# Kernel tuning notes

Hardware: AMD Instinct MI355X
Metric: run time of the kernel (lower is better)

## Reference

```python
import jax, jax.numpy as jnp
import numpy as np

N_NODES = 100000
N_EDGES = 1600000
N_GRAPHS = 128
IN_F, H_F, OUT_F, HID, NCLS = 128, 128, 64, 10, 10

def setup_inputs() -> dict:
    key = jax.random.key(0)
    ks = jax.random.split(key, 12)
    feats = jax.random.normal(ks[0], (N_NODES, IN_F), dtype=jnp.float32)
    src = jax.random.randint(ks[1], (N_EDGES,), 0, N_NODES, dtype=jnp.int32)
    dst = jax.random.randint(ks[2], (N_EDGES,), 0, N_NODES, dtype=jnp.int32)
    graph_ids = jnp.sort(jax.random.randint(ks[3], (N_NODES,), 0, N_GRAPHS, dtype=jnp.int32))
    def glorot(k, shape):
        fan = shape[0] + shape[1]
        return jax.random.normal(k, shape, dtype=jnp.float32) * jnp.sqrt(2.0 / fan)
    return {
        'feats': feats, 'src': src, 'dst': dst, 'graph_ids': graph_ids,
        'W1': glorot(ks[4], (IN_F, H_F)), 'b1': jnp.zeros((H_F,), jnp.float32),
        'W2': glorot(ks[5], (H_F, OUT_F)), 'b2': jnp.zeros((OUT_F,), jnp.float32),
        'fcW1': glorot(ks[6], (OUT_F, HID)), 'fcb1': jnp.zeros((HID,), jnp.float32),
        'fcW2': glorot(ks[7], (HID, NCLS)), 'fcb2': jnp.zeros((NCLS,), jnp.float32),
    }

def _graph_conv(x, W, b, src, dst):
    # DGL GraphConv, norm='both': D_dst^{-1/2} A D_src^{-1/2} X W + b
    ones = jnp.ones((src.shape[0],), x.dtype)
    deg_out = jnp.clip(jax.ops.segment_sum(ones, src, num_segments=N_NODES), 1.0)
    deg_in = jnp.clip(jax.ops.segment_sum(ones, dst, num_segments=N_NODES), 1.0)
    x = x * jax.lax.rsqrt(deg_out)[:, None]
    m = jax.ops.segment_sum(x[src], dst, num_segments=N_NODES)  # gather-scatter over edges
    m = m * jax.lax.rsqrt(deg_in)[:, None]
    return m @ W + b

def reference(feats, src, dst, graph_ids, W1, b1, W2, b2, fcW1, fcb1, fcW2, fcb2):
    h = jax.nn.relu(_graph_conv(feats, W1, b1, src, dst))
    h = jax.nn.relu(_graph_conv(h, W2, b2, src, dst))
    # dgl.mean_nodes: per-graph mean pooling
    sums = jax.ops.segment_sum(h, graph_ids, num_segments=N_GRAPHS)
    counts = jnp.clip(jax.ops.segment_sum(jnp.ones((N_NODES,), h.dtype), graph_ids, num_segments=N_GRAPHS), 1.0)
    pooled = sums / counts[:, None]  # [G, OUT_F]
    z = jax.nn.relu(pooled @ fcW1 + fcb1)
    return jax.nn.softmax(z @ fcW2 + fcb2, axis=1)
```

## Files before the change

kernel.cpp:

```cpp
#include <hip/hip_runtime.h>
#include <hip/hip_bf16.h>

#define N_NODES 100000
#define N_EDGES 1600000
#define N_GRAPHS 128
#define IN_F 128
#define H_F 128
#define OUT_F 64
#define HID 10
#define NCLS 10
#define XPAD 136
#define BSH 7
#define NBUCK 782
#define SBLK 128
#define EPB (N_EDGES / SBLK)
#define NB_PREP 4
#define PCHUNK 8

typedef __attribute__((ext_vector_type(8))) short bf16x8;
typedef __attribute__((ext_vector_type(4))) float f32x4;
typedef __attribute__((ext_vector_type(2))) float f32x2;

__device__ __forceinline__ float bl(unsigned int u) { return __uint_as_float(u << 16); }
__device__ __forceinline__ float bh(unsigned int u) { return __uint_as_float(u & 0xffff0000u); }

__global__ __launch_bounds__(1024) void k_hist2(const int* __restrict__ src, const int* __restrict__ dst,
                                                int* __restrict__ Pd, int* __restrict__ Ps,
                                                const float* __restrict__ W1, const float* __restrict__ W2,
                                                unsigned short* __restrict__ Wt1, unsigned short* __restrict__ Wt2) {
    __shared__ int hd[NBUCK];
    __shared__ int hs[NBUCK];
    const int blk = blockIdx.x;
    if (blk < SBLK) {
        for (int i = threadIdx.x; i < NBUCK; i += 1024) { hd[i] = 0; hs[i] = 0; }
        __syncthreads();
        const int base = blk * EPB;
        for (int i = threadIdx.x; i < EPB; i += 1024) {
            atomicAdd(&hd[dst[base + i] >> BSH], 1);
            atomicAdd(&hs[src[base + i] >> BSH], 1);
        }
        __syncthreads();
        for (int b = threadIdx.x; b < NBUCK; b += 1024) {
            Pd[b * SBLK + blk] = hd[b];
            Ps[b * SBLK + blk] = hs[b];
        }
    } else {
        int t = (blk - SBLK) * 1024 + threadIdx.x;
        const int stride = NB_PREP * 1024;
        for (int i = t; i < 128 * 128; i += stride) {
            int c = i >> 7, k = i & 127;
            __hip_bfloat16 v = __float2bfloat16(W1[k * 128 + c]);
            Wt1[i] = *(unsigned short*)&v;
        }
        for (int i = t; i < 64 * 128; i += stride) {
            int c = i >> 7, k = i & 127;
            __hip_bfloat16 v = __float2bfloat16(W2[k * 64 + c]);
            Wt2[i] = *(unsigned short*)&v;
        }
    }
}

__global__ __launch_bounds__(SBLK) void k_scanA(int* __restrict__ Pd, int* __restrict__ Ps,
                                                int* __restrict__ Td, int* __restrict__ Ts) {
    __shared__ int sc[SBLK];
    const int b = blockIdx.x;
    const int t = threadIdx.x;
    int* P = (b < NBUCK) ? Pd : Ps;
    int* T = (b < NBUCK) ? Td : Ts;
    const int bb = (b < NBUCK) ? b : b - NBUCK;
    int v = P[bb * SBLK + t];
    sc[t] = v;
    __syncthreads();
    for (int off = 1; off < SBLK; off <<= 1) {
        int u = (t >= off) ? sc[t - off] : 0;
        __syncthreads();
        sc[t] += u;
        __syncthreads();
    }
    P[bb * SBLK + t] = sc[t] - v;
    if (t == SBLK - 1) T[bb] = sc[SBLK - 1];
}

__global__ __launch_bounds__(1024) void k_scanB(const int* __restrict__ Td, const int* __restrict__ Ts,
                                                int* __restrict__ Bd, int* __restrict__ Bs) {
    __shared__ int sc[1024];
    const int t = threadIdx.x;
    int v = (t < NBUCK) ? Td[t] : 0;
    sc[t] = v;
    __syncthreads();
    for (int off = 1; off < 1024; off <<= 1) {
        int u = (t >= off) ? sc[t - off] : 0;
        __syncthreads();
        sc[t] += u;
        __syncthreads();
    }
    if (t < NBUCK) Bd[t] = sc[t] - v;
    if (t == NBUCK - 1) Bd[NBUCK] = sc[t];
    __syncthreads();
    int v2 = (t < NBUCK) ? Ts[t] : 0;
    sc[t] = v2;
    __syncthreads();
    for (int off = 1; off < 1024; off <<= 1) {
        int u = (t >= off) ? sc[t - off] : 0;
        __syncthreads();
        sc[t] += u;
        __syncthreads();
    }
    if (t < NBUCK) Bs[t] = sc[t] - v2;
    if (t == NBUCK - 1) Bs[NBUCK] = sc[t];
}

__global__ __launch_bounds__(1024) void k_scatter(const int* __restrict__ src, const int* __restrict__ dst,
                                                  const int* __restrict__ Pd, const int* __restrict__ Ps,
                                                  const int* __restrict__ Bd, const int* __restrict__ Bs,
                                                  unsigned int* __restrict__ pb, unsigned char* __restrict__ sb) {
    __shared__ int tk[NBUCK];
    const int b = blockIdx.x;
    const bool isPb = b < SBLK;
    const int blk = isPb ? b : b - SBLK;
    if (isPb) {
        for (int i = threadIdx.x; i < NBUCK; i += 1024) tk[i] = Bd[i] + Pd[i * SBLK + blk];
    } else {
        for (int i = threadIdx.x; i < NBUCK; i += 1024) tk[i] = Bs[i] + Ps[i * SBLK + blk];
    }
    __syncthreads();
    const int base = blk * EPB;
    if (isPb) {
        for (int i = threadIdx.x; i < EPB; i += 1024) {
            int d = dst[base + i];
            int s = src[base + i];
            int bd = d >> BSH;
            int pos = atomicAdd(&tk[bd], 1);
            pb[pos] = ((unsigned)s << 7) | (unsigned)(d & 127);
        }
    } else {
        for (int i = threadIdx.x; i < EPB; i += 1024) {
            int s = src[base + i];
            int bs = s >> BSH;
            int pos = atomicAdd(&tk[bs], 1);
            sb[pos] = (unsigned char)(s & 127);
        }
    }
}

__global__ __launch_bounds__(256) void k_finalize(const unsigned int* __restrict__ pb, const int* __restrict__ Bd,
                                                  const unsigned char* __restrict__ sb, const int* __restrict__ Bs,
                                                  int* __restrict__ rp, int* __restrict__ cnt_out,
                                                  int* __restrict__ cols) {
    __shared__ int cnt[128];
    __shared__ int exc[128];
    __shared__ int tick[128];
    __shared__ int h[128];
    __shared__ int sc[128];
    const int b = blockIdx.x;
    const int tid = threadIdx.x;
    if (tid < 128) { cnt[tid] = 0; tick[tid] = 0; h[tid] = 0; }
    __syncthreads();
    const int e0 = Bd[b], e1 = Bd[b + 1];
    for (int i = e0 + tid; i < e1; i += 256) atomicAdd(&cnt[pb[i] & 127], 1);
    const int f0 = Bs[b], f1 = Bs[b + 1];
    for (int i = f0 + tid; i < f1; i += 256) atomicAdd(&h[sb[i]], 1);
    __syncthreads();
    if (tid < 128) sc[tid] = cnt[tid];
    __syncthreads();
    for (int off = 1; off < 128; off <<= 1) {
        int u = (tid < 128 && tid >= off) ? sc[tid - off] : 0;
        __syncthreads();
        if (tid < 128) sc[tid] += u;
        __syncthreads();
    }
    if (tid < 128) exc[tid] = sc[tid] - cnt[tid];
    __syncthreads();
    const int node0 = b << BSH;
    if (tid < 128 && node0 + tid < N_NODES) {
        rp[node0 + tid] = e0 + exc[tid];
        cnt_out[node0 + tid] = h[tid];
    }
    if (b == NBUCK - 1 && tid == 0) rp[N_NODES] = N_EDGES;
    for (int i = e0 + tid; i < e1; i += 256) {
        unsigned int p = pb[i];
        int loc = p & 127;
        int t = atomicAdd(&tick[loc], 1);
        cols[e0 + exc[loc] + t] = (int)(p >> 7);
    }
}

__global__ __launch_bounds__(256) void k_gemm1(const float* __restrict__ X,
                                               const unsigned short* __restrict__ Wt,
                                               const int* __restrict__ cnt_out,
                                               unsigned char* __restrict__ Gout) {
    __shared__ __align__(16) unsigned short Xs[32 * XPAD];
    __shared__ __align__(16) unsigned short Ws[128 * XPAD];
    const int tid = threadIdx.x;
    const int row0 = blockIdx.x * 32;

    {
        const float4* X4 = (const float4*)X;
#pragma unroll
        for (int j = 0; j < 4; j++) {
            int i = tid + 256 * j;
            int r = i >> 5, k4 = i & 31;
            float4 x = X4[(size_t)(row0 + r) * 32 + k4];
            __hip_bfloat162 lo = __float22bfloat162_rn({x.x, x.y});
            __hip_bfloat162 hi = __float22bfloat162_rn({x.z, x.w});
            uint2 u;
            u.x = *(unsigned int*)&lo;
            u.y = *(unsigned int*)&hi;
            *(uint2*)&Xs[r * XPAD + k4 * 4] = u;
        }
    }
    {
        const uint2* W2 = (const uint2*)Wt;
#pragma unroll
        for (int j = 0; j < 16; j++) {
            int i = tid + 256 * j;
            int cc = i >> 5, kk = i & 31;
            uint2 u = W2[(size_t)cc * 32 + kk];
            *(uint2*)&Ws[cc * XPAD + kk * 4] = u;
        }
    }
    __syncthreads();

    const int lane = tid & 63;
    const int wv = tid >> 6;
    const int m = lane & 15;
    const int q = lane >> 4;
    const int cg = wv * 32;

    f32x4 acc00 = {0.f, 0.f, 0.f, 0.f}, acc01 = {0.f, 0.f, 0.f, 0.f};
    f32x4 acc10 = {0.f, 0.f, 0.f, 0.f}, acc11 = {0.f, 0.f, 0.f, 0.f};
#pragma unroll
    for (int ks = 0; ks < 4; ks++) {
        int kb = ks * 32 + q * 8;
        bf16x8 a0 = *(const bf16x8*)&Xs[m * XPAD + kb];
        bf16x8 a1 = *(const bf16x8*)&Xs[(16 + m) * XPAD + kb];
        bf16x8 b0 = *(const bf16x8*)&Ws[(cg + m) * XPAD + kb];
        bf16x8 b1 = *(const bf16x8*)&Ws[(cg + 16 + m) * XPAD + kb];
        acc00 = __builtin_amdgcn_mfma_f32_16x16x32_bf16(a0, b0, acc00, 0, 0, 0);
        acc01 = __builtin_amdgcn_mfma_f32_16x16x32_bf16(a0, b1, acc01, 0, 0, 0);
        acc10 = __builtin_amdgcn_mfma_f32_16x16x32_bf16(a1, b0, acc10, 0, 0, 0);
        acc11 = __builtin_amdgcn_mfma_f32_16x16x32_bf16(a1, b1, acc11, 0, 0, 0);
    }
#pragma unroll
    for (int r = 0; r < 4; r++) {
        int rowA = row0 + q * 4 + r;
        int rowB = rowA + 16;
        float sA = rsqrtf((float)max(cnt_out[rowA], 1));
        float sB = rsqrtf((float)max(cnt_out[rowB], 1));
        unsigned int pkA = __builtin_amdgcn_cvt_pk_fp8_f32(acc00[r] * sA, acc01[r] * sA, 0, false);
        unsigned int pkB = __builtin_amdgcn_cvt_pk_fp8_f32(acc10[r] * sB, acc11[r] * sB, 0, false);
        unsigned char* gA = Gout + (size_t)rowA * 128 + cg + m;
        gA[0]  = (unsigned char)(pkA & 0xffu);
        gA[16] = (unsigned char)((pkA >> 8) & 0xffu);
        unsigned char* gB = Gout + (size_t)rowB * 128 + cg + m;
        gB[0]  = (unsigned char)(pkB & 0xffu);
        gB[16] = (unsigned char)((pkB >> 8) & 0xffu);
    }
}

template <int TOTF, bool XBF16, bool OUT_FP8>
__global__ __launch_bounds__(256) void k_gemm_mfma(const void* __restrict__ Xv,
                                                   const unsigned short* __restrict__ Wt,
                                                   const int* __restrict__ cnt_out,
                                                   void* __restrict__ GoutV) {
    __shared__ __align__(16) unsigned short Xs[32 * XPAD];
    __shared__ __align__(16) unsigned short Ws[64 * XPAD];
    const int tid = threadIdx.x;
    const int cbase = blockIdx.y * 64;
    const int row0 = blockIdx.x * 32;

    if constexpr (XBF16) {
        const uint2* X2 = (const uint2*)Xv;
#pragma unroll
        for (int j = 0; j < 4; j++) {
            int i = tid + 256 * j;
            int r = i >> 5, kk = i & 31;
            uint2 u = X2[(size_t)(row0 + r) * 32 + kk];
            *(uint2*)&Xs[r * XPAD + kk * 4] = u;
        }
    } else {
        const float4* X4 = (const float4*)Xv;
#pragma unroll
        for (int j = 0; j < 4; j++) {
            int i = tid + 256 * j;
            int r = i >> 5, k4 = i & 31;
            float4 x = X4[(size_t)(row0 + r) * 32 + k4];
            __hip_bfloat162 lo = __float22bfloat162_rn({x.x, x.y});
            __hip_bfloat162 hi = __float22bfloat162_rn({x.z, x.w});
            uint2 u;
            u.x = *(unsigned int*)&lo;
            u.y = *(unsigned int*)&hi;
            *(uint2*)&Xs[r * XPAD + k4 * 4] = u;
        }
    }
    {
        const uint2* W2 = (const uint2*)Wt;
#pragma unroll
        for (int j = 0; j < 8; j++) {
            int i = tid + 256 * j;
            int c = i >> 5, kk = i & 31;
            uint2 u = W2[(size_t)(cbase + c) * 32 + kk];
            *(uint2*)&Ws[c * XPAD + kk * 4] = u;
        }
    }
    __syncthreads();

    const int lane = tid & 63;
    const int wv = tid >> 6;
    const int m = lane & 15;
    const int q = lane >> 4;
    const int roff = (wv & 1) * 16;
    const int coff = (wv >> 1) * 32;

    f32x4 acc0 = {0.f, 0.f, 0.f, 0.f}, acc1 = {0.f, 0.f, 0.f, 0.f};
#pragma unroll
    for (int ks = 0; ks < 4; ks++) {
        int kb = ks * 32 + q * 8;
        bf16x8 a  = *(const bf16x8*)&Xs[(roff + m) * XPAD + kb];
        bf16x8 b0 = *(const bf16x8*)&Ws[(coff + m) * XPAD + kb];
        bf16x8 b1 = *(const bf16x8*)&Ws[(coff + 16 + m) * XPAD + kb];
        acc0 = __builtin_amdgcn_mfma_f32_16x16x32_bf16(a, b0, acc0, 0, 0, 0);
        acc1 = __builtin_amdgcn_mfma_f32_16x16x32_bf16(a, b1, acc1, 0, 0, 0);
    }
#pragma unroll
    for (int r = 0; r < 4; r++) {
        int row = row0 + roff + q * 4 + r;
        float s = rsqrtf((float)max(cnt_out[row], 1));
        int col0 = cbase + coff + m;
        if constexpr (OUT_FP8) {
            unsigned int pk = __builtin_amdgcn_cvt_pk_fp8_f32(acc0[r] * s, acc1[r] * s, 0, false);
            unsigned char* gp = (unsigned char*)GoutV + (size_t)row * TOTF + col0;
            gp[0]  = (unsigned char)(pk & 0xffu);
            gp[16] = (unsigned char)((pk >> 8) & 0xffu);
        } else {
            unsigned short* Gout = (unsigned short*)GoutV;
            __hip_bfloat16 o0 = __float2bfloat16(acc0[r] * s);
            __hip_bfloat16 o1 = __float2bfloat16(acc1[r] * s);
            Gout[(size_t)row * TOTF + col0]      = *(unsigned short*)&o0;
            Gout[(size_t)row * TOTF + col0 + 16] = *(unsigned short*)&o1;
        }
    }
}

__device__ __forceinline__ void tail128(const unsigned short* __restrict__ gl, const int* __restrict__ cols,
                                        int b, int d, int j, f32x2& acc) {
    while (j + 16 <= d) {
        unsigned int u[16];
#pragma unroll
        for (int k = 0; k < 16; k++) { int s = cols[b + j + k]; u[k] = gl[(size_t)s * 64]; }
#pragma unroll
        for (int k = 0; k < 16; k++) acc += __builtin_amdgcn_cvt_pk_f32_fp8(u[k], false);
        j += 16;
    }
    if (j + 8 <= d) {
        unsigned int u[8];
#pragma unroll
        for (int k = 0; k < 8; k++) { int s = cols[b + j + k]; u[k] = gl[(size_t)s * 64]; }
#pragma unroll
        for (int k = 0; k < 8; k++) acc += __builtin_amdgcn_cvt_pk_f32_fp8(u[k], false);
        j += 8;
    }
    if (j + 4 <= d) {
        unsigned int u[4];
#pragma unroll
        for (int k = 0; k < 4; k++) { int s = cols[b + j + k]; u[k] = gl[(size_t)s * 64]; }
#pragma unroll
        for (int k = 0; k < 4; k++) acc += __builtin_amdgcn_cvt_pk_f32_fp8(u[k], false);
        j += 4;
    }
    if (j + 2 <= d) {
        unsigned int u0, u1;
        { int s = cols[b + j];     u0 = gl[(size_t)s * 64]; }
        { int s = cols[b + j + 1]; u1 = gl[(size_t)s * 64]; }
        acc += __builtin_amdgcn_cvt_pk_f32_fp8(u0, false);
        acc += __builtin_amdgcn_cvt_pk_f32_fp8(u1, false);
        j += 2;
    }
    if (j < d) {
        int s = cols[b + j];
        unsigned int u = gl[(size_t)s * 64];
        acc += __builtin_amdgcn_cvt_pk_f32_fp8(u, false);
    }
}

__device__ __forceinline__ void tail64(const unsigned char* __restrict__ gl, const int* __restrict__ cols,
                                       int b, int d, int j, f32x2& acc) {
    while (j + 16 <= d) {
        unsigned int u[16];
#pragma unroll
        for (int k = 0; k < 16; k++) { int s = cols[b + j + k]; u[k] = gl[(size_t)s * 64]; }
#pragma unroll
        for (int k = 0; k < 16; k++) acc += __builtin_amdgcn_cvt_pk_f32_fp8(u[k], false);
        j += 16;
    }
    if (j + 8 <= d) {
        unsigned int u[8];
#pragma unroll
        for (int k = 0; k < 8; k++) { int s = cols[b + j + k]; u[k] = gl[(size_t)s * 64]; }
#pragma unroll
        for (int k = 0; k < 8; k++) acc += __builtin_amdgcn_cvt_pk_f32_fp8(u[k], false);
        j += 8;
    }
    if (j + 4 <= d) {
        unsigned int u[4];
#pragma unroll
        for (int k = 0; k < 4; k++) { int s = cols[b + j + k]; u[k] = gl[(size_t)s * 64]; }
#pragma unroll
        for (int k = 0; k < 4; k++) acc += __builtin_amdgcn_cvt_pk_f32_fp8(u[k], false);
        j += 4;
    }
    if (j + 2 <= d) {
        unsigned int u0, u1;
        { int s = cols[b + j];     u0 = gl[(size_t)s * 64]; }
        { int s = cols[b + j + 1]; u1 = gl[(size_t)s * 64]; }
        acc += __builtin_amdgcn_cvt_pk_f32_fp8(u0, false);
        acc += __builtin_amdgcn_cvt_pk_f32_fp8(u1, false);
        j += 2;
    }
    if (j < d) {
        int s = cols[b + j];
        unsigned int u = gl[(size_t)s * 64];
        acc += __builtin_amdgcn_cvt_pk_f32_fp8(u, false);
    }
}

__global__ __launch_bounds__(256) void k_spmm128f8(const unsigned short* __restrict__ G,
                                                   const int* __restrict__ rp,
                                                   const int* __restrict__ cols,
                                                   const float* __restrict__ bias,
                                                   unsigned int* __restrict__ H) {
    const int lane = threadIdx.x & 63;
    const int wave = threadIdx.x >> 6;
    const int v0 = (blockIdx.x * 4 + wave) * 2;
    const int b0 = __builtin_amdgcn_readfirstlane(rp[v0]);
    const int b1 = __builtin_amdgcn_readfirstlane(rp[v0 + 1]);
    const int e1 = __builtin_amdgcn_readfirstlane(rp[v0 + 2]);
    const int dA = b1 - b0, dB = e1 - b1;
    const unsigned short* gl = G + lane;
    f32x2 aA = {0.f, 0.f}, aB = {0.f, 0.f};
    int ja = 0, jb = 0;
    while (ja + 8 <= dA && jb + 8 <= dB) {
        unsigned int u[8], w[8];
#pragma unroll
        for (int k = 0; k < 8; k++) { int s = cols[b0 + ja + k]; u[k] = gl[(size_t)s * 64]; }
#pragma unroll
        for (int k = 0; k < 8; k++) { int s = cols[b1 + jb + k]; w[k] = gl[(size_t)s * 64]; }
#pragma unroll
        for (int k = 0; k < 8; k++) aA += __builtin_amdgcn_cvt_pk_f32_fp8(u[k], false);
#pragma unroll
        for (int k = 0; k < 8; k++) aB += __builtin_amdgcn_cvt_pk_f32_fp8(w[k], false);
        ja += 8; jb += 8;
    }
    tail128(gl, cols, b0, dA, ja, aA);
    tail128(gl, cols, b1, dB, jb, aB);

    {
        const float rs = rsqrtf((float)max(dA, 1));
        const float2 bb = *(const float2*)&bias[2 * lane];
        __hip_bfloat162 p = __float22bfloat162_rn({fmaxf(fmaf(aA.x, rs, bb.x), 0.f),
                                                   fmaxf(fmaf(aA.y, rs, bb.y), 0.f)});
        H[(size_t)v0 * 64 + lane] = *(unsigned int*)&p;
    }
    {
        const float rs = rsqrtf((float)max(dB, 1));
        const float2 bb = *(const float2*)&bias[2 * lane];
        __hip_bfloat162 p = __float22bfloat162_rn({fmaxf(fmaf(aB.x, rs, bb.x), 0.f),
                                                   fmaxf(fmaf(aB.y, rs, bb.y), 0.f)});
        H[(size_t)(v0 + 1) * 64 + lane] = *(unsigned int*)&p;
    }
}

__global__ __launch_bounds__(256) void k_spmm64f8(const unsigned char* __restrict__ G,
                                                  const int* __restrict__ rp,
                                                  const int* __restrict__ cols,
                                                  const float* __restrict__ bias,
                                                  unsigned short* __restrict__ H) {
    const int lane = threadIdx.x & 63;
    const int wave = threadIdx.x >> 6;
    const int v0 = (blockIdx.x * 4 + wave) * 2;
    const int b0 = __builtin_amdgcn_readfirstlane(rp[v0]);
    const int b1 = __builtin_amdgcn_readfirstlane(rp[v0 + 1]);
    const int e1 = __builtin_amdgcn_readfirstlane(rp[v0 + 2]);
    const int dA = b1 - b0, dB = e1 - b1;
    const unsigned char* gl = G + lane;
    f32x2 aA = {0.f, 0.f}, aB = {0.f, 0.f};
    int ja = 0, jb = 0;
    while (ja + 8 <= dA && jb + 8 <= dB) {
        unsigned int u[8], w[8];
#pragma unroll
        for (int k = 0; k < 8; k++) { int s = cols[b0 + ja + k]; u[k] = gl[(size_t)s * 64]; }
#pragma unroll
        for (int k = 0; k < 8; k++) { int s = cols[b1 + jb + k]; w[k] = gl[(size_t)s * 64]; }
#pragma unroll
        for (int k = 0; k < 8; k++) aA += __builtin_amdgcn_cvt_pk_f32_fp8(u[k], false);
#pragma unroll
        for (int k = 0; k < 8; k++) aB += __builtin_amdgcn_cvt_pk_f32_fp8(w[k], false);
        ja += 8; jb += 8;
    }
    tail64(gl, cols, b0, dA, ja, aA);
    tail64(gl, cols, b1, dB, jb, aB);

    {
        const float rs = rsqrtf((float)max(dA, 1));
        __hip_bfloat16 o = __float2bfloat16(fmaxf(fmaf(aA.x, rs, bias[lane]), 0.f));
        H[(size_t)v0 * 64 + lane] = *(unsigned short*)&o;
    }
    {
        const float rs = rsqrtf((float)max(dB, 1));
        __hip_bfloat16 o = __float2bfloat16(fmaxf(fmaf(aB.x, rs, bias[lane]), 0.f));
        H[(size_t)(v0 + 1) * 64 + lane] = *(unsigned short*)&o;
    }
}

__global__ __launch_bounds__(256) void k_pool(const unsigned short* __restrict__ h2,
                                              const int* __restrict__ gid,
                                              float* __restrict__ part) {
    __shared__ int se[2];
    __shared__ float red[16][16][4];
    const int cpart = blockIdx.x;
    const int g = blockIdx.y;
    const int tid = threadIdx.x;
    if (tid < 2) {
        int target = g + tid;
        int lo = 0, hi = N_NODES;
        while (lo < hi) {
            int mid = (lo + hi) >> 1;
            if (gid[mid] < target) lo = mid + 1; else hi = mid;
        }
        se[tid] = lo;
    }
    __syncthreads();
    const int s = se[0], e = se[1];
    const int chunk = (e - s + PCHUNK - 1) / PCHUNK;
    const int lo = s + cpart * chunk;
    const int hi = min(lo + chunk, e);
    const int r = tid >> 4, cp = tid & 15;
    float a0 = 0.f, a1 = 0.f, a2 = 0.f, a3 = 0.f;
    const uint2* H = (const uint2*)h2;
    for (int v = lo + r; v < hi; v += 16) {
        uint2 u = H[(size_t)v * 16 + cp];
        a0 += bl(u.x); a1 += bh(u.x); a2 += bl(u.y); a3 += bh(u.y);
    }
    red[r][cp][0] = a0; red[r][cp][1] = a1; red[r][cp][2] = a2; red[r][cp][3] = a3;
    for (int off = 8; off > 0; off >>= 1) {
        __syncthreads();
        if (r < off) {
#pragma unroll
            for (int k = 0; k < 4; k++) red[r][cp][k] += red[r + off][cp][k];
        }
    }
    __syncthreads();
    if (r == 0) {
        float4 o = {red[0][cp][0], red[0][cp][1], red[0][cp][2], red[0][cp][3]};
        *(float4*)&part[((size_t)cpart * N_GRAPHS + g) * 64 + 4 * cp] = o;
    }
}

__global__ __launch_bounds__(64) void k_mlp(const float* __restrict__ part,
                                            const int* __restrict__ gid,
                                            const float* __restrict__ fcW1,
                                            const float* __restrict__ fcb1,
                                            const float* __restrict__ fcW2,
                                            const float* __restrict__ fcb2,
                                            float* __restrict__ out) {
    __shared__ int se[2];
    __shared__ float p[64];
    __shared__ float z[10];
    __shared__ float l[10];
    __shared__ float red[2];
    const int g = blockIdx.x;
    const int t = threadIdx.x;
    if (t < 2) {
        int target = g + t;
        int lo = 0, hi = N_NODES;
        while (lo < hi) {
            int mid = (lo + hi) >> 1;
            if (gid[mid] < target) lo = mid + 1; else hi = mid;
        }
        se[t] = lo;
    }
    __syncthreads();
    const int cnt = max(se[1] - se[0], 1);
    float a = 0.f;
#pragma unroll
    for (int c = 0; c < PCHUNK; c++) a += part[((size_t)c * N_GRAPHS + g) * 64 + t];
    p[t] = a / (float)cnt;
    __syncthreads();
    if (t < 10) {
        float acc = fcb1[t];
        for (int k = 0; k < 64; k++) acc = fmaf(p[k], fcW1[k * 10 + t], acc);
        z[t] = fmaxf(acc, 0.f);
    }
    __syncthreads();
    if (t < 10) {
        float acc = fcb2[t];
        for (int k = 0; k < 10; k++) acc = fmaf(z[k], fcW2[k * 10 + t], acc);
        l[t] = acc;
    }
    __syncthreads();
    if (t == 0) {
        float m = l[0];
        for (int i = 1; i < 10; i++) m = fmaxf(m, l[i]);
        float ssum = 0.f;
        for (int i = 0; i < 10; i++) ssum += expf(l[i] - m);
        red[0] = m;
        red[1] = ssum;
    }
    __syncthreads();
    if (t < 10) out[g * 10 + t] = expf(l[t] - red[0]) / red[1];
}

extern "C" void kernel_launch(void* const* d_in, const int* in_sizes, int n_in,
                              void* d_out, int out_size, void* d_ws, size_t ws_size,
                              hipStream_t stream) {
    const float* feats = (const float*)d_in[0];
    const int* src = (const int*)d_in[1];
    const int* dst = (const int*)d_in[2];
    const int* gid = (const int*)d_in[3];
    const float* W1 = (const float*)d_in[4];
    const float* b1 = (const float*)d_in[5];
    const float* W2 = (const float*)d_in[6];
    const float* b2 = (const float*)d_in[7];
    const float* fcW1 = (const float*)d_in[8];
    const float* fcb1 = (const float*)d_in[9];
    const float* fcW2 = (const float*)d_in[10];
    const float* fcb2 = (const float*)d_in[11];
    float* out = (float*)d_out;

    char* w = (char*)d_ws;
    size_t off = 0;
    auto alloc = [&](size_t bytes) -> void* {
        void* p = w + off;
        off = (off + bytes + 255) & ~(size_t)255;
        return p;
    };
    int* cnt_out = (int*)alloc(N_NODES * 4);
    int* rp      = (int*)alloc((N_NODES + 1) * 4);
    int* cols    = (int*)alloc((size_t)N_EDGES * 4);
    int* Pd      = (int*)alloc(NBUCK * SBLK * 4);
    int* Ps      = (int*)alloc(NBUCK * SBLK * 4);
    int* Td      = (int*)alloc(NBUCK * 4);
    int* Ts      = (int*)alloc(NBUCK * 4);
    int* Bd      = (int*)alloc((NBUCK + 1) * 4);
    int* Bs      = (int*)alloc((NBUCK + 1) * 4);
    unsigned int* pb  = (unsigned int*)alloc((size_t)N_EDGES * 4);
    unsigned char* sb = (unsigned char*)alloc((size_t)N_EDGES);
    unsigned short* Wt1 = (unsigned short*)alloc(128 * 128 * 2);
    unsigned short* Wt2 = (unsigned short*)alloc(64 * 128 * 2);
    unsigned char* g1 = (unsigned char*)alloc((size_t)N_NODES * 128);
    unsigned short* h1 = (unsigned short*)alloc((size_t)N_NODES * 128 * 2);
    unsigned char* g2 = (unsigned char*)alloc((size_t)N_NODES * 64);
    unsigned short* h2 = (unsigned short*)alloc((size_t)N_NODES * 64 * 2);
    float* part = (float*)alloc((size_t)PCHUNK * N_GRAPHS * 64 * 4);

    k_hist2<<<SBLK + NB_PREP, 1024, 0, stream>>>(src, dst, Pd, Ps, W1, W2, Wt1, Wt2);
    k_scanA<<<2 * NBUCK, SBLK, 0, stream>>>(Pd, Ps, Td, Ts);
    k_scanB<<<1, 1024, 0, stream>>>(Td, Ts, Bd, Bs);
    k_scatter<<<2 * SBLK, 1024, 0, stream>>>(src, dst, Pd, Ps, Bd, Bs, pb, sb);
    k_finalize<<<NBUCK, 256, 0, stream>>>(pb, Bd, sb, Bs, rp, cnt_out, cols);

    k_gemm1<<<N_NODES / 32, 256, 0, stream>>>(feats, Wt1, cnt_out, g1);
    k_spmm128f8<<<N_NODES / 8, 256, 0, stream>>>((const unsigned short*)g1, rp, cols, b1, (unsigned int*)h1);

    k_gemm_mfma<64, true, true><<<dim3(N_NODES / 32, 1), 256, 0, stream>>>(h1, Wt2, cnt_out, g2);
    k_spmm64f8<<<N_NODES / 8, 256, 0, stream>>>(g2, rp, cols, b2, (unsigned short*)h2);

    k_pool<<<dim3(PCHUNK, N_GRAPHS), 256, 0, stream>>>(h2, gid, part);
    k_mlp<<<N_GRAPHS, 64, 0, stream>>>(part, gid, fcW1, fcb1, fcW2, fcb2, out);
}
```

Measured before the change: 260.5 us.

## Fuse mean-pool partial sums into layer-2 SpMM with atomics

The second SpMM kernel now reduces its eight output rows per block into per-graph sums in shared memory and atomically adds them into a single fp32 partial buffer. This removes the bf16 h2 write and read and the separate pooling kernel launch. The partial buffer is zeroed in the first prep kernel. The cost is 12500 blocks issuing float atomics onto a small buffer, which adds contention and makes the summation order nondeterministic.

```diff
diff --git a/kernel.cpp b/kernel.cpp
--- a/kernel.cpp
+++ b/kernel.cpp
@@ -15,7 +15,6 @@
 #define SBLK 128
 #define EPB (N_EDGES / SBLK)
 #define NB_PREP 4
-#define PCHUNK 8
 
 typedef __attribute__((ext_vector_type(8))) short bf16x8;
 typedef __attribute__((ext_vector_type(4))) float f32x4;
@@ -27,7 +26,8 @@
 __global__ __launch_bounds__(1024) void k_hist2(const int* __restrict__ src, const int* __restrict__ dst,
                                                 int* __restrict__ Pd, int* __restrict__ Ps,
                                                 const float* __restrict__ W1, const float* __restrict__ W2,
-                                                unsigned short* __restrict__ Wt1, unsigned short* __restrict__ Wt2) {
+                                                unsigned short* __restrict__ Wt1, unsigned short* __restrict__ Wt2,
+                                                float* __restrict__ part) {
     __shared__ int hd[NBUCK];
     __shared__ int hs[NBUCK];
     const int blk = blockIdx.x;
@@ -57,6 +57,7 @@
             __hip_bfloat16 v = __float2bfloat16(W2[k * 64 + c]);
             Wt2[i] = *(unsigned short*)&v;
         }
+        for (int i = t; i < N_GRAPHS * 64; i += stride) part[i] = 0.f;
     }
 }
 
@@ -474,15 +475,20 @@
                                                   const int* __restrict__ rp,
                                                   const int* __restrict__ cols,
                                                   const float* __restrict__ bias,
-                                                  unsigned short* __restrict__ H) {
+                                                  const int* __restrict__ gid,
+                                                  float* __restrict__ part) {
+    __shared__ float acc[8][64];
+    __shared__ int gv[8];
     const int lane = threadIdx.x & 63;
     const int wave = threadIdx.x >> 6;
-    const int v0 = (blockIdx.x * 4 + wave) * 2;
+    const int vb = blockIdx.x * 8;
+    const int v0 = vb + wave * 2;
     const int b0 = __builtin_amdgcn_readfirstlane(rp[v0]);
     const int b1 = __builtin_amdgcn_readfirstlane(rp[v0 + 1]);
     const int e1 = __builtin_amdgcn_readfirstlane(rp[v0 + 2]);
     const int dA = b1 - b0, dB = e1 - b1;
     const unsigned char* gl = G + lane;
+    if (threadIdx.x < 8) gv[threadIdx.x] = gid[vb + threadIdx.x];
     f32x2 aA = {0.f, 0.f}, aB = {0.f, 0.f};
     int ja = 0, jb = 0;
     while (ja + 8 <= dA && jb + 8 <= dB) {
@@ -500,59 +506,33 @@
     tail64(gl, cols, b0, dA, ja, aA);
     tail64(gl, cols, b1, dB, jb, aB);
 
+    const float bbias = bias[lane];
     {
         const float rs = rsqrtf((float)max(dA, 1));
-        __hip_bfloat16 o = __float2bfloat16(fmaxf(fmaf(aA.x, rs, bias[lane]), 0.f));
-        H[(size_t)v0 * 64 + lane] = *(unsigned short*)&o;
+        acc[wave * 2][lane] = fmaxf(fmaf(aA.x, rs, bbias), 0.f);
     }
     {
         const float rs = rsqrtf((float)max(dB, 1));
-        __hip_bfloat16 o = __float2bfloat16(fmaxf(fmaf(aB.x, rs, bias[lane]), 0.f));
-        H[(size_t)(v0 + 1) * 64 + lane] = *(unsigned short*)&o;
-    }
-}
-
-__global__ __launch_bounds__(256) void k_pool(const unsigned short* __restrict__ h2,
-                                              const int* __restrict__ gid,
-                                              float* __restrict__ part) {
-    __shared__ int se[2];
-    __shared__ float red[16][16][4];
-    const int cpart = blockIdx.x;
-    const int g = blockIdx.y;
-    const int tid = threadIdx.x;
-    if (tid < 2) {
-        int target = g + tid;
-        int lo = 0, hi = N_NODES;
-        while (lo < hi) {
-            int mid = (lo + hi) >> 1;
-            if (gid[mid] < target) lo = mid + 1; else hi = mid;
-        }
-        se[tid] = lo;
-    }
-    __syncthreads();
-    const int s = se[0], e = se[1];
-    const int chunk = (e - s + PCHUNK - 1) / PCHUNK;
-    const int lo = s + cpart * chunk;
-    const int hi = min(lo + chunk, e);
-    const int r = tid >> 4, cp = tid & 15;
-    float a0 = 0.f, a1 = 0.f, a2 = 0.f, a3 = 0.f;
-    const uint2* H = (const uint2*)h2;
-    for (int v = lo + r; v < hi; v += 16) {
-        uint2 u = H[(size_t)v * 16 + cp];
-        a0 += bl(u.x); a1 += bh(u.x); a2 += bl(u.y); a3 += bh(u.y);
-    }
-    red[r][cp][0] = a0; red[r][cp][1] = a1; red[r][cp][2] = a2; red[r][cp][3] = a3;
-    for (int off = 8; off > 0; off >>= 1) {
-        __syncthreads();
-        if (r < off) {
-#pragma unroll
-            for (int k = 0; k < 4; k++) red[r][cp][k] += red[r + off][cp][k];
-        }
-    }
-    __syncthreads();
-    if (r == 0) {
-        float4 o = {red[0][cp][0], red[0][cp][1], red[0][cp][2], red[0][cp][3]};
-        *(float4*)&part[((size_t)cpart * N_GRAPHS + g) * 64 + 4 * cp] = o;
+        acc[wave * 2 + 1][lane] = fmaxf(fmaf(aB.x, rs, bbias), 0.f);
+    }
+    __syncthreads();
+    if (threadIdx.x < 64) {
+        const int col = threadIdx.x;
+        float sum = acc[0][col];
+        int g = gv[0];
+#pragma unroll
+        for (int r = 1; r < 8; r++) {
+            int gr = gv[r];
+            float v = acc[r][col];
+            if (gr != g) {
+                atomicAdd(&part[g * 64 + col], sum);
+                sum = v;
+                g = gr;
+            } else {
+                sum += v;
+            }
+        }
+        atomicAdd(&part[g * 64 + col], sum);
     }
 }
 
@@ -581,10 +561,7 @@
     }
     __syncthreads();
     const int cnt = max(se[1] - se[0], 1);
-    float a = 0.f;
-#pragma unroll
-    for (int c = 0; c < PCHUNK; c++) a += part[((size_t)c * N_GRAPHS + g) * 64 + t];
-    p[t] = a / (float)cnt;
+    p[t] = part[g * 64 + t] / (float)cnt;
     __syncthreads();
     if (t < 10) {
         float acc = fcb1[t];
@@ -650,10 +627,9 @@
     unsigned char* g1 = (unsigned char*)alloc((size_t)N_NODES * 128);
     unsigned short* h1 = (unsigned short*)alloc((size_t)N_NODES * 128 * 2);
     unsigned char* g2 = (unsigned char*)alloc((size_t)N_NODES * 64);
-    unsigned short* h2 = (unsigned short*)alloc((size_t)N_NODES * 64 * 2);
-    float* part = (float*)alloc((size_t)PCHUNK * N_GRAPHS * 64 * 4);
-
-    k_hist2<<<SBLK + NB_PREP, 1024, 0, stream>>>(src, dst, Pd, Ps, W1, W2, Wt1, Wt2);
+    float* part = (float*)alloc((size_t)N_GRAPHS * 64 * 4);
+
+    k_hist2<<<SBLK + NB_PREP, 1024, 0, stream>>>(src, dst, Pd, Ps, W1, W2, Wt1, Wt2, part);
     k_scanA<<<2 * NBUCK, SBLK, 0, stream>>>(Pd, Ps, Td, Ts);
     k_scanB<<<1, 1024, 0, stream>>>(Td, Ts, Bd, Bs);
     k_scatter<<<2 * SBLK, 1024, 0, stream>>>(src, dst, Pd, Ps, Bd, Bs, pb, sb);
@@ -663,8 +639,7 @@
     k_spmm128f8<<<N_NODES / 8, 256, 0, stream>>>((const unsigned short*)g1, rp, cols, b1, (unsigned int*)h1);
 
     k_gemm_mfma<64, true, true><<<dim3(N_NODES / 32, 1), 256, 0, stream>>>(h1, Wt2, cnt_out, g2);
-    k_spmm64f8<<<N_NODES / 8, 256, 0, stream>>>(g2, rp, cols, b2, (unsigned short*)h2);
-
-    k_pool<<<dim3(PCHUNK, N_GRAPHS), 256, 0, stream>>>(h2, gid, part);
+    k_spmm64f8<<<N_NODES / 8, 256, 0, stream>>>(g2, rp, cols, b2, gid, part);
+
     k_mlp<<<N_GRAPHS, 64, 0, stream>>>(part, gid, fcW1, fcb1, fcW2, fcb2, out);
 }
```

New measurement: 258.7 us (median of 2 runs). Within noise of the previous version (-0.7%).
